# Kernel tuning notes

Hardware: AMD Instinct MI355X
Metric: run time of the kernel (lower is better)

Reference implementation:

```python
import jax, jax.numpy as jnp
import numpy as np

N_NODES = 100000
N_EDGES = 1600000
IN_CH = 128
HID_CH = 128


def setup_inputs() -> dict:
    key = jax.random.key(0)
    ks = jax.random.split(key, 10)
    x = jax.random.normal(ks[0], (N_NODES, IN_CH), dtype=jnp.float32)
    edge_index = jax.random.randint(ks[1], (2, N_EDGES), 0, N_NODES, dtype=jnp.int64)
    s1 = 1.0 / np.sqrt(IN_CH)
    s2 = 1.0 / np.sqrt(HID_CH)
    return {
        "x": x,
        "edge_index": edge_index,
        "W1": jax.random.uniform(ks[2], (IN_CH, HID_CH), jnp.float32, -s1, s1),
        "b1": jnp.zeros((HID_CH,), jnp.float32),
        "W2": jax.random.uniform(ks[3], (HID_CH, HID_CH), jnp.float32, -s2, s2),
        "b2": jnp.zeros((HID_CH,), jnp.float32),
        "We": jax.random.uniform(ks[4], (IN_CH, HID_CH), jnp.float32, -s1, s1),
        "be": jax.random.uniform(ks[5], (HID_CH,), jnp.float32, -s1, s1),
        "Wfc": jax.random.uniform(ks[6], (HID_CH, 1), jnp.float32, -s2, s2),
        "bfc": jax.random.uniform(ks[7], (1,), jnp.float32, -s2, s2),
    }


def _gcn_conv(x, src, dst, norm, W, b, n_nodes):
    # PyG GCNConv: linear transform, then normalized scatter-add aggregation, then bias
    h = x @ W                                 # [N, H]
    msg = h[src] * norm[:, None]              # gather + scale  [E+N, H]
    out = jax.ops.segment_sum(msg, dst, num_segments=n_nodes)  # scatter-add [N, H]
    return out + b


def reference(x, edge_index, W1, b1, W2, b2, We, be, Wfc, bfc):
    n = x.shape[0]
    # add self-loops (PyG default add_self_loops=True)
    loop = jnp.arange(n, dtype=edge_index.dtype)
    src = jnp.concatenate([edge_index[0], loop])
    dst = jnp.concatenate([edge_index[1], loop])
    # symmetric degree normalization deg^-1/2 (edge_weight implicitly ones)
    deg = jax.ops.segment_sum(jnp.ones_like(src, dtype=x.dtype), dst, num_segments=n)
    dinv = jnp.where(deg > 0, jax.lax.rsqrt(deg), 0.0)
    norm = dinv[src] * dinv[dst]

    x_conv = jax.nn.relu(_gcn_conv(x, src, dst, norm, W1, b1, n))
    x_fc = jax.nn.relu(x @ We + be)
    h = x_conv + x_fc                          # residual; dropout is identity in eval
    x_conv2 = jax.nn.relu(_gcn_conv(h, src, dst, norm, W2, b2, n))
    h = x_conv2 + h
    # batch is all zeros -> global_mean_pool == mean over all nodes -> [1, H]
    pooled = jnp.mean(h, axis=0, keepdims=True)
    predict = jax.nn.sigmoid(pooled @ Wfc + bfc)  # [1, 1]
    return predict
```

## Files before the change

kernel.cpp:

```cpp
#include <hip/hip_runtime.h>
#include <hip/hip_bf16.h>

typedef unsigned int uint;
typedef unsigned short ushort;
typedef unsigned char uchar;
typedef __attribute__((ext_vector_type(8))) short short8;
typedef __attribute__((ext_vector_type(4))) float f32x4;
typedef __attribute__((ext_vector_type(4))) uint u32x4;

__device__ __forceinline__ float bf2f(ushort u) {
    union { uint i; float f; } v; v.i = ((uint)u) << 16; return v.f;
}
__device__ __forceinline__ ushort f2bf(float f) {
    union { float f; uint i; } v; v.f = f;
    uint x = v.i;
    uint r = (x + 0x7FFFu + ((x >> 16) & 1u)) >> 16;
    return (ushort)r;
}
__device__ __forceinline__ uchar f2q(float f) {
    return (uchar)(__builtin_amdgcn_cvt_pk_fp8_f32(f, 0.f, 0, false) & 0xFF);
}
__device__ __forceinline__ void q2f4(uint w, float* o) {
    o[0] = __builtin_amdgcn_cvt_f32_fp8(w, 0);
    o[1] = __builtin_amdgcn_cvt_f32_fp8(w, 1);
    o[2] = __builtin_amdgcn_cvt_f32_fp8(w, 2);
    o[3] = __builtin_amdgcn_cvt_f32_fp8(w, 3);
}


__global__ void k_degree(const int* __restrict__ dst, int* __restrict__ deg,
                         int e, int n) {
    int bin = blockIdx.x & 7;
    int sub = blockIdx.x >> 3;
    int nsub = gridDim.x >> 3;
    int q = (n + 7) >> 3;
    int lo = bin * q, hi = min(n, lo + q);
    for (int i = sub * 256 + threadIdx.x; i < e; i += nsub * 256) {
        int d = dst[i];
        if (d >= lo && d < hi) atomicAdd(&deg[d], 1);
    }
}

__global__ void k_dinv(const int* __restrict__ deg, float* __restrict__ dinv, int n) {
    int i = blockIdx.x * 256 + threadIdx.x;
    if (i < n) dinv[i] = rsqrtf((float)deg[i] + 1.0f);
}

__global__ void k_scan_a(const int* __restrict__ deg, int* __restrict__ bsum, int n) {
    __shared__ int sd[256];
    int t = threadIdx.x;
    int base = blockIdx.x * 1024 + t * 4;
    int s = 0;
#pragma unroll
    for (int j = 0; j < 4; ++j) { int idx = base + j; if (idx < n) s += deg[idx]; }
    sd[t] = s; __syncthreads();
    for (int off = 1; off < 256; off <<= 1) {
        int v = (t >= off) ? sd[t - off] : 0;
        __syncthreads();
        sd[t] += v;
        __syncthreads();
    }
    if (t == 255) bsum[blockIdx.x] = sd[255];
}

__global__ void k_scan_b(const int* __restrict__ bsum, int* __restrict__ boff, int nb) {
    __shared__ int sd[256];
    int t = threadIdx.x;
    int v0 = (t < nb) ? bsum[t] : 0;
    sd[t] = v0; __syncthreads();
    for (int off = 1; off < 256; off <<= 1) {
        int v = (t >= off) ? sd[t - off] : 0;
        __syncthreads();
        sd[t] += v;
        __syncthreads();
    }
    if (t < nb) boff[t] = sd[t] - v0;
}

__global__ void k_scan_c(const int* __restrict__ deg, const int* __restrict__ boff,
                         int* __restrict__ offs, int n) {
    __shared__ int sd[256];
    int t = threadIdx.x;
    int base = blockIdx.x * 1024 + t * 4;
    int vals[4]; int s = 0;
#pragma unroll
    for (int j = 0; j < 4; ++j) {
        int idx = base + j;
        vals[j] = (idx < n) ? deg[idx] : 0;
        s += vals[j];
    }
    sd[t] = s; __syncthreads();
    for (int off = 1; off < 256; off <<= 1) {
        int v = (t >= off) ? sd[t - off] : 0;
        __syncthreads();
        sd[t] += v;
        __syncthreads();
    }
    int run = boff[blockIdx.x] + (sd[t] - s);
#pragma unroll
    for (int j = 0; j < 4; ++j) {
        int idx = base + j;
        if (idx < n) { offs[idx] = run; run += vals[j]; }
    }
}

__global__ void k_fill(const int* __restrict__ src, const int* __restrict__ dst,
                       const int* __restrict__ offs, int* __restrict__ cursor,
                       int* __restrict__ csr, int e, int n) {
    int bin = blockIdx.x & 7;
    int sub = blockIdx.x >> 3;
    int nsub = gridDim.x >> 3;
    int q = (n + 7) >> 3;
    int lo = bin * q, hi = min(n, lo + q);
    for (int i = sub * 256 + threadIdx.x; i < e; i += nsub * 256) {
        int d = dst[i];
        if (d >= lo && d < hi) {
            int p = offs[d] + atomicAdd(&cursor[d], 1);
            csr[p] = src[i];
        }
    }
}


__global__ __launch_bounds__(512) void k_gemm1(
    const float* __restrict__ x, const float* __restrict__ W1, const float* __restrict__ We,
    const float* __restrict__ be, const float* __restrict__ dinv,
    uchar* __restrict__ h1q, ushort* __restrict__ xfc, int n)
{
    __shared__ __align__(16) ushort Bt[256][72];
    int tid = threadIdx.x;
    int w = tid >> 6, lane = tid & 63;
    int ln15 = lane & 15, g = lane >> 4;
    int rowBase = blockIdx.x * 128 + w * 16;
    int r = rowBase + ln15;
    bool valid = r < n;

    short8 a[4];
#pragma unroll
    for (int ks = 0; ks < 4; ++ks) {
        float4 f0 = make_float4(0.f, 0.f, 0.f, 0.f), f1 = f0;
        if (valid) {
            const float* p = x + (size_t)r * 128 + ks * 32 + g * 8;
            f0 = *reinterpret_cast<const float4*>(p);
            f1 = *reinterpret_cast<const float4*>(p + 4);
        }
        short8 v;
        v[0] = (short)f2bf(f0.x); v[1] = (short)f2bf(f0.y);
        v[2] = (short)f2bf(f0.z); v[3] = (short)f2bf(f0.w);
        v[4] = (short)f2bf(f1.x); v[5] = (short)f2bf(f1.y);
        v[6] = (short)f2bf(f1.z); v[7] = (short)f2bf(f1.w);
        a[ks] = v;
    }

    f32x4 acc[16];
#pragma unroll
    for (int i = 0; i < 16; ++i) acc[i] = (f32x4){0.f, 0.f, 0.f, 0.f};

    for (int s = 0; s < 2; ++s) {
        for (int i = tid; i < 8192; i += 512) {
            int kl = i >> 7, j = i & 127;
            int kg = s * 64 + kl;
            Bt[j][kl]       = f2bf(W1[kg * 128 + j]);
            Bt[128 + j][kl] = f2bf(We[kg * 128 + j]);
        }
        __syncthreads();
#pragma unroll
        for (int t2 = 0; t2 < 2; ++t2) {
            short8 af = a[s * 2 + t2];
#pragma unroll
            for (int jf = 0; jf < 16; ++jf) {
                short8 bf = *reinterpret_cast<const short8*>(&Bt[jf * 16 + ln15][t2 * 32 + g * 8]);
                acc[jf] = __builtin_amdgcn_mfma_f32_16x16x32_bf16(af, bf, acc[jf], 0, 0, 0);
            }
        }
        __syncthreads();
    }

    float dv[4];
#pragma unroll
    for (int q = 0; q < 4; ++q) {
        int rr = rowBase + g * 4 + q;
        dv[q] = (rr < n) ? dinv[rr] : 0.f;
    }

#pragma unroll
    for (int jf = 0; jf < 16; ++jf) {
        int col = jf * 16 + ln15;
#pragma unroll
        for (int q = 0; q < 4; ++q) {
            int rr = rowBase + g * 4 + q;
            if (rr < n) {
                float v = acc[jf][q];
                if (col < 128) {
                    h1q[(size_t)rr * 128 + col] = f2q(v * dv[q]);
                } else {
                    float vv = fmaxf(v + be[col - 128], 0.f);
                    xfc[(size_t)rr * 128 + (col - 128)] = f2bf(vv);
                }
            }
        }
    }
}


__global__ __launch_bounds__(512) void k_gemm2(
    const ushort* __restrict__ h, const float* __restrict__ W2, const float* __restrict__ dinv,
    uchar* __restrict__ h2q, int n)
{
    __shared__ __align__(16) ushort Bt[128][72];
    int tid = threadIdx.x;
    int w = tid >> 6, lane = tid & 63;
    int ln15 = lane & 15, g = lane >> 4;
    int rowBase = blockIdx.x * 128 + w * 16;
    int r = rowBase + ln15;
    bool valid = r < n;

    short8 a[4];
#pragma unroll
    for (int ks = 0; ks < 4; ++ks) {
        short8 v = (short8){0,0,0,0,0,0,0,0};
        if (valid) v = *reinterpret_cast<const short8*>(h + (size_t)r * 128 + ks * 32 + g * 8);
        a[ks] = v;
    }

    f32x4 acc[8];
#pragma unroll
    for (int i = 0; i < 8; ++i) acc[i] = (f32x4){0.f, 0.f, 0.f, 0.f};

    for (int s = 0; s < 2; ++s) {
        for (int i = tid; i < 8192; i += 512) {
            int kl = i >> 7, j = i & 127;
            Bt[j][kl] = f2bf(W2[(s * 64 + kl) * 128 + j]);
        }
        __syncthreads();
#pragma unroll
        for (int t2 = 0; t2 < 2; ++t2) {
            short8 af = a[s * 2 + t2];
#pragma unroll
            for (int jf = 0; jf < 8; ++jf) {
                short8 bf = *reinterpret_cast<const short8*>(&Bt[jf * 16 + ln15][t2 * 32 + g * 8]);
                acc[jf] = __builtin_amdgcn_mfma_f32_16x16x32_bf16(af, bf, acc[jf], 0, 0, 0);
            }
        }
        __syncthreads();
    }

    float dv[4];
#pragma unroll
    for (int q = 0; q < 4; ++q) {
        int rr = rowBase + g * 4 + q;
        dv[q] = (rr < n) ? dinv[rr] : 0.f;
    }

#pragma unroll
    for (int jf = 0; jf < 8; ++jf) {
        int col = jf * 16 + ln15;
#pragma unroll
        for (int q = 0; q < 4; ++q) {
            int rr = rowBase + g * 4 + q;
            if (rr < n) h2q[(size_t)rr * 128 + col] = f2q(acc[jf][q] * dv[q]);
        }
    }
}


__global__ __launch_bounds__(256) void k_agg1(
    const int* __restrict__ csr, const int* __restrict__ offs, const int* __restrict__ degE,
    const float* __restrict__ dinv, const uchar* __restrict__ h1q, const ushort* __restrict__ xfc,
    const float* __restrict__ b1, ushort* __restrict__ h, int n)
{
    int t = threadIdx.x;
    int g = t >> 3, li = t & 7;
    int node = blockIdx.x * 32 + g;
    if (node >= n) return;
    int off = offs[node], cnt = degE[node];
    float di = dinv[node];
    int c0 = li * 16;
    const uchar* tbl = h1q + c0;
    float acc[16];
#pragma unroll
    for (int e = 0; e < 16; ++e) acc[e] = 0.f;

    for (int base = 0; base < cnt; base += 16) {
        int idx[16];
#pragma unroll
        for (int q = 0; q < 16; ++q) {
            int s = csr[off + base + q];
            idx[q] = (base + q < cnt) ? s : n;
        }
        u32x4 u[16];
#pragma unroll
        for (int q = 0; q < 16; ++q)
            u[q] = *reinterpret_cast<const u32x4*>(tbl + (size_t)idx[q] * 128);
#pragma unroll
        for (int q = 0; q < 16; ++q) {
            float d4[4];
            q2f4(u[q][0], d4); acc[0] += d4[0]; acc[1] += d4[1]; acc[2] += d4[2]; acc[3] += d4[3];
            q2f4(u[q][1], d4); acc[4] += d4[0]; acc[5] += d4[1]; acc[6] += d4[2]; acc[7] += d4[3];
            q2f4(u[q][2], d4); acc[8] += d4[0]; acc[9] += d4[1]; acc[10] += d4[2]; acc[11] += d4[3];
            q2f4(u[q][3], d4); acc[12] += d4[0]; acc[13] += d4[1]; acc[14] += d4[2]; acc[15] += d4[3];
        }
    }

    u32x4 us = *reinterpret_cast<const u32x4*>(tbl + (size_t)node * 128);
    float sdec[16];
    q2f4(us[0], sdec); q2f4(us[1], sdec + 4); q2f4(us[2], sdec + 8); q2f4(us[3], sdec + 12);
    const u32x4* xp = reinterpret_cast<const u32x4*>(xfc + (size_t)node * 128 + c0);
    u32x4 x0 = xp[0], x1 = xp[1];
    uint xw[8] = {x0[0], x0[1], x0[2], x0[3], x1[0], x1[1], x1[2], x1[3]};
    float bb[16];
#pragma unroll
    for (int p = 0; p < 4; ++p) {
        float4 bq = *reinterpret_cast<const float4*>(b1 + c0 + p * 4);
        bb[4 * p] = bq.x; bb[4 * p + 1] = bq.y; bb[4 * p + 2] = bq.z; bb[4 * p + 3] = bq.w;
    }
    uint outw[8];
#pragma unroll
    for (int j = 0; j < 8; ++j) {
        int e0 = 2 * j, e1 = 2 * j + 1;
        float v0 = fmaxf((acc[e0] + sdec[e0]) * di + bb[e0], 0.f) + bf2f((ushort)(xw[j] & 0xffff));
        float v1 = fmaxf((acc[e1] + sdec[e1]) * di + bb[e1], 0.f) + bf2f((ushort)(xw[j] >> 16));
        outw[j] = (uint)f2bf(v0) | ((uint)f2bf(v1) << 16);
    }
    ushort* hp = h + (size_t)node * 128 + c0;
    u32x4 o0 = {outw[0], outw[1], outw[2], outw[3]};
    u32x4 o1 = {outw[4], outw[5], outw[6], outw[7]};
    *reinterpret_cast<u32x4*>(hp) = o0;
    *reinterpret_cast<u32x4*>(hp + 8) = o1;
}


__global__ __launch_bounds__(256) void k_agg2(
    const int* __restrict__ csr, const int* __restrict__ offs, const int* __restrict__ degE,
    const float* __restrict__ dinv, const uchar* __restrict__ h2q, const ushort* __restrict__ hres,
    const float* __restrict__ b2, float* __restrict__ pooled, int n)
{
    __shared__ float lpool[128];
    int t = threadIdx.x;
    if (t < 128) lpool[t] = 0.f;
    __syncthreads();
    int g = t >> 3, li = t & 7;
    int node = blockIdx.x * 32 + g;
    bool valid = node < n;
    int nodeC = valid ? node : (n - 1);
    int off = offs[nodeC];
    int cnt = valid ? degE[nodeC] : 0;
    float di = dinv[nodeC];
    int c0 = li * 16;
    const uchar* tbl = h2q + c0;
    float acc[16];
#pragma unroll
    for (int e = 0; e < 16; ++e) acc[e] = 0.f;

    for (int base = 0; base < cnt; base += 16) {
        int idx[16];
#pragma unroll
        for (int q = 0; q < 16; ++q) {
            int s = csr[off + base + q];
            idx[q] = (base + q < cnt) ? s : n;
        }
        u32x4 u[16];
#pragma unroll
        for (int q = 0; q < 16; ++q)
            u[q] = *reinterpret_cast<const u32x4*>(tbl + (size_t)idx[q] * 128);
#pragma unroll
        for (int q = 0; q < 16; ++q) {
            float d4[4];
            q2f4(u[q][0], d4); acc[0] += d4[0]; acc[1] += d4[1]; acc[2] += d4[2]; acc[3] += d4[3];
            q2f4(u[q][1], d4); acc[4] += d4[0]; acc[5] += d4[1]; acc[6] += d4[2]; acc[7] += d4[3];
            q2f4(u[q][2], d4); acc[8] += d4[0]; acc[9] += d4[1]; acc[10] += d4[2]; acc[11] += d4[3];
            q2f4(u[q][3], d4); acc[12] += d4[0]; acc[13] += d4[1]; acc[14] += d4[2]; acc[15] += d4[3];
        }
    }

    u32x4 us = *reinterpret_cast<const u32x4*>(tbl + (size_t)nodeC * 128);
    float sdec[16];
    q2f4(us[0], sdec); q2f4(us[1], sdec + 4); q2f4(us[2], sdec + 8); q2f4(us[3], sdec + 12);
    const u32x4* rp = reinterpret_cast<const u32x4*>(hres + (size_t)nodeC * 128 + c0);
    u32x4 r0 = rp[0], r1 = rp[1];
    uint rw[8] = {r0[0], r0[1], r0[2], r0[3], r1[0], r1[1], r1[2], r1[3]};
    float bb[16];
#pragma unroll
    for (int p = 0; p < 4; ++p) {
        float4 bq = *reinterpret_cast<const float4*>(b2 + c0 + p * 4);
        bb[4 * p] = bq.x; bb[4 * p + 1] = bq.y; bb[4 * p + 2] = bq.z; bb[4 * p + 3] = bq.w;
    }
    if (valid) {
#pragma unroll
        for (int j = 0; j < 8; ++j) {
            int e0 = 2 * j, e1 = 2 * j + 1;
            float v0 = fmaxf((acc[e0] + sdec[e0]) * di + bb[e0], 0.f) + bf2f((ushort)(rw[j] & 0xffff));
            float v1 = fmaxf((acc[e1] + sdec[e1]) * di + bb[e1], 0.f) + bf2f((ushort)(rw[j] >> 16));
            atomicAdd(&lpool[c0 + e0], v0);
            atomicAdd(&lpool[c0 + e1], v1);
        }
    }
    __syncthreads();
    if (t < 128) atomicAdd(&pooled[t], lpool[t]);
}


__global__ void k_final(const float* __restrict__ pooled, const float* __restrict__ Wfc,
                        const float* __restrict__ bfc, float* __restrict__ out, float invN) {
    int lane = threadIdx.x;
    float s = pooled[2 * lane] * invN * Wfc[2 * lane] +
              pooled[2 * lane + 1] * invN * Wfc[2 * lane + 1];
#pragma unroll
    for (int off = 32; off > 0; off >>= 1) s += __shfl_down(s, off);
    if (lane == 0) out[0] = 1.f / (1.f + expf(-(s + bfc[0])));
}


extern "C" void kernel_launch(void* const* d_in, const int* in_sizes, int n_in,
                              void* d_out, int out_size, void* d_ws, size_t ws_size,
                              hipStream_t stream) {
    const float* x   = (const float*)d_in[0];
    const int*   ei  = (const int*)d_in[1];
    const float* W1  = (const float*)d_in[2];
    const float* b1  = (const float*)d_in[3];
    const float* W2  = (const float*)d_in[4];
    const float* b2  = (const float*)d_in[5];
    const float* We  = (const float*)d_in[6];
    const float* be  = (const float*)d_in[7];
    const float* Wfc = (const float*)d_in[8];
    const float* bfc = (const float*)d_in[9];
    float* out = (float*)d_out;

    const int N = in_sizes[0] / 128;
    const int E = in_sizes[1] / 2;
    const int* src = ei;
    const int* dst = ei + E;

    char* w = (char*)d_ws;
    size_t off = 0;
    auto take = [&](size_t bytes) -> void* {
        void* p = w + off;
        off = (off + bytes + 255) & ~(size_t)255;
        return p;
    };
    int*    deg    = (int*)take((size_t)N * 4);
    int*    offs   = (int*)take((size_t)N * 4);
    int*    cursor = (int*)take((size_t)N * 4);
    float*  dinv   = (float*)take((size_t)N * 4);
    int*    bsum   = (int*)take(1024);
    int*    boff   = (int*)take(1024);
    int*    csr    = (int*)take((size_t)(E + 64) * 4);
    uchar*  h1q    = (uchar*)take((size_t)(N + 1) * 128);
    ushort* xfc    = (ushort*)take((size_t)N * 128 * 2);
    ushort* h      = (ushort*)take((size_t)N * 128 * 2);
    uchar*  h2q    = (uchar*)take((size_t)(N + 1) * 128);
    float*  pooled = (float*)take(512);

    const int nbScan = (N + 1023) / 1024;

    hipMemsetAsync(deg, 0, (size_t)N * 4, stream);
    hipMemsetAsync(cursor, 0, (size_t)N * 4, stream);
    hipMemsetAsync(pooled, 0, 512, stream);
    hipMemsetAsync(h1q + (size_t)N * 128, 0, 128, stream);
    hipMemsetAsync(h2q + (size_t)N * 128, 0, 128, stream);

    k_degree<<<2048, 256, 0, stream>>>(dst, deg, E, N);
    k_dinv<<<(N + 255) / 256, 256, 0, stream>>>(deg, dinv, N);
    k_scan_a<<<nbScan, 256, 0, stream>>>(deg, bsum, N);
    k_scan_b<<<1, 256, 0, stream>>>(bsum, boff, nbScan);
    k_scan_c<<<nbScan, 256, 0, stream>>>(deg, boff, offs, N);
    k_fill<<<2048, 256, 0, stream>>>(src, dst, offs, cursor, csr, E, N);

    k_gemm1<<<(N + 127) / 128, 512, 0, stream>>>(x, W1, We, be, dinv, h1q, xfc, N);
    k_agg1<<<(N + 31) / 32, 256, 0, stream>>>(csr, offs, deg, dinv, h1q, xfc, b1, h, N);
    k_gemm2<<<(N + 127) / 128, 512, 0, stream>>>(h, W2, dinv, h2q, N);
    k_agg2<<<(N + 31) / 32, 256, 0, stream>>>(csr, offs, deg, dinv, h2q, h, b2, pooled, N);
    k_final<<<1, 64, 0, stream>>>(pooled, Wfc, bfc, out, 1.0f / (float)N);
}
```

Baseline: 423.6 us.

## Sort nodes by degree for load-balanced aggregation and fuse memsets into init kernel

Adds a degree histogram, a scan and a scatter that build a degree-sorted node order. Both aggregation kernels then process nodes in that order, so the 8-thread groups in a wavefront have similar edge counts and less divergence. The gather batch drops from 16 to 8 neighbours, and the five memsets are replaced by one init kernel. The cost is three extra small launches, scattered output writes, and less memory-level parallelism per batch.

```diff
diff --git a/kernel.cpp b/kernel.cpp
--- a/kernel.cpp
+++ b/kernel.cpp
@@ -25,6 +25,21 @@
     o[1] = __builtin_amdgcn_cvt_f32_fp8(w, 1);
     o[2] = __builtin_amdgcn_cvt_f32_fp8(w, 2);
     o[3] = __builtin_amdgcn_cvt_f32_fp8(w, 3);
+}
+
+
+__global__ void k_init(int* __restrict__ deg, int* __restrict__ cursor,
+                       int* __restrict__ hist, int* __restrict__ cursB,
+                       float* __restrict__ pooled,
+                       uchar* __restrict__ h1qN, uchar* __restrict__ h2qN, int n) {
+    int i = blockIdx.x * 256 + threadIdx.x;
+    if (i < n) { deg[i] = 0; cursor[i] = 0; }
+    if (i < 64) { hist[i] = 0; cursB[i] = 0; }
+    if (i < 128) pooled[i] = 0.f;
+    if (i < 32) {
+        reinterpret_cast<uint*>(h1qN)[i] = 0;
+        reinterpret_cast<uint*>(h2qN)[i] = 0;
+    }
 }
 
 
@@ -122,6 +137,36 @@
 }
 
 
+__global__ void k_hist(const int* __restrict__ deg, int* __restrict__ hist, int n) {
+    int i = blockIdx.x * 256 + threadIdx.x;
+    if (i < n) atomicAdd(&hist[min(deg[i], 63)], 1);
+}
+
+__global__ void k_sortscan(const int* __restrict__ hist, int* __restrict__ base) {
+    __shared__ int sd[64];
+    int t = threadIdx.x;
+    int v0 = hist[t];
+    sd[t] = v0; __syncthreads();
+    for (int off = 1; off < 64; off <<= 1) {
+        int v = (t >= off) ? sd[t - off] : 0;
+        __syncthreads();
+        sd[t] += v;
+        __syncthreads();
+    }
+    base[t] = sd[t] - v0;
+}
+
+__global__ void k_scatter(const int* __restrict__ deg, const int* __restrict__ base,
+                          int* __restrict__ cursB, int* __restrict__ order, int n) {
+    int i = blockIdx.x * 256 + threadIdx.x;
+    if (i < n) {
+        int b = min(deg[i], 63);
+        int pos = base[b] + atomicAdd(&cursB[b], 1);
+        order[pos] = i;
+    }
+}
+
+
 __global__ __launch_bounds__(512) void k_gemm1(
     const float* __restrict__ x, const float* __restrict__ W1, const float* __restrict__ We,
     const float* __restrict__ be, const float* __restrict__ dinv,
@@ -267,12 +312,13 @@
 __global__ __launch_bounds__(256) void k_agg1(
     const int* __restrict__ csr, const int* __restrict__ offs, const int* __restrict__ degE,
     const float* __restrict__ dinv, const uchar* __restrict__ h1q, const ushort* __restrict__ xfc,
-    const float* __restrict__ b1, ushort* __restrict__ h, int n)
+    const float* __restrict__ b1, ushort* __restrict__ h, const int* __restrict__ order, int n)
 {
     int t = threadIdx.x;
     int g = t >> 3, li = t & 7;
-    int node = blockIdx.x * 32 + g;
-    if (node >= n) return;
+    int j = blockIdx.x * 32 + g;
+    if (j >= n) return;
+    int node = order[j];
     int off = offs[node], cnt = degE[node];
     float di = dinv[node];
     int c0 = li * 16;
@@ -281,19 +327,16 @@
 #pragma unroll
     for (int e = 0; e < 16; ++e) acc[e] = 0.f;
 
-    for (int base = 0; base < cnt; base += 16) {
-        int idx[16];
-#pragma unroll
-        for (int q = 0; q < 16; ++q) {
+    for (int base = 0; base < cnt; base += 8) {
+        u32x4 u[8];
+#pragma unroll
+        for (int q = 0; q < 8; ++q) {
             int s = csr[off + base + q];
-            idx[q] = (base + q < cnt) ? s : n;
-        }
-        u32x4 u[16];
-#pragma unroll
-        for (int q = 0; q < 16; ++q)
-            u[q] = *reinterpret_cast<const u32x4*>(tbl + (size_t)idx[q] * 128);
-#pragma unroll
-        for (int q = 0; q < 16; ++q) {
+            int id = (base + q < cnt) ? s : n;
+            u[q] = *reinterpret_cast<const u32x4*>(tbl + (size_t)id * 128);
+        }
+#pragma unroll
+        for (int q = 0; q < 8; ++q) {
             float d4[4];
             q2f4(u[q][0], d4); acc[0] += d4[0]; acc[1] += d4[1]; acc[2] += d4[2]; acc[3] += d4[3];
             q2f4(u[q][1], d4); acc[4] += d4[0]; acc[5] += d4[1]; acc[6] += d4[2]; acc[7] += d4[3];
@@ -316,11 +359,11 @@
     }
     uint outw[8];
 #pragma unroll
-    for (int j = 0; j < 8; ++j) {
-        int e0 = 2 * j, e1 = 2 * j + 1;
-        float v0 = fmaxf((acc[e0] + sdec[e0]) * di + bb[e0], 0.f) + bf2f((ushort)(xw[j] & 0xffff));
-        float v1 = fmaxf((acc[e1] + sdec[e1]) * di + bb[e1], 0.f) + bf2f((ushort)(xw[j] >> 16));
-        outw[j] = (uint)f2bf(v0) | ((uint)f2bf(v1) << 16);
+    for (int jj = 0; jj < 8; ++jj) {
+        int e0 = 2 * jj, e1 = 2 * jj + 1;
+        float v0 = fmaxf((acc[e0] + sdec[e0]) * di + bb[e0], 0.f) + bf2f((ushort)(xw[jj] & 0xffff));
+        float v1 = fmaxf((acc[e1] + sdec[e1]) * di + bb[e1], 0.f) + bf2f((ushort)(xw[jj] >> 16));
+        outw[jj] = (uint)f2bf(v0) | ((uint)f2bf(v1) << 16);
     }
     ushort* hp = h + (size_t)node * 128 + c0;
     u32x4 o0 = {outw[0], outw[1], outw[2], outw[3]};
@@ -333,38 +376,35 @@
 __global__ __launch_bounds__(256) void k_agg2(
     const int* __restrict__ csr, const int* __restrict__ offs, const int* __restrict__ degE,
     const float* __restrict__ dinv, const uchar* __restrict__ h2q, const ushort* __restrict__ hres,
-    const float* __restrict__ b2, float* __restrict__ pooled, int n)
+    const float* __restrict__ b2, float* __restrict__ pooled, const int* __restrict__ order, int n)
 {
     __shared__ float lpool[128];
     int t = threadIdx.x;
     if (t < 128) lpool[t] = 0.f;
     __syncthreads();
     int g = t >> 3, li = t & 7;
-    int node = blockIdx.x * 32 + g;
-    bool valid = node < n;
-    int nodeC = valid ? node : (n - 1);
-    int off = offs[nodeC];
-    int cnt = valid ? degE[nodeC] : 0;
-    float di = dinv[nodeC];
+    int j = blockIdx.x * 32 + g;
+    bool valid = j < n;
+    int node = valid ? order[j] : 0;
+    int off = offs[node];
+    int cnt = valid ? degE[node] : 0;
+    float di = dinv[node];
     int c0 = li * 16;
     const uchar* tbl = h2q + c0;
     float acc[16];
 #pragma unroll
     for (int e = 0; e < 16; ++e) acc[e] = 0.f;
 
-    for (int base = 0; base < cnt; base += 16) {
-        int idx[16];
-#pragma unroll
-        for (int q = 0; q < 16; ++q) {
+    for (int base = 0; base < cnt; base += 8) {
+        u32x4 u[8];
+#pragma unroll
+        for (int q = 0; q < 8; ++q) {
             int s = csr[off + base + q];
-            idx[q] = (base + q < cnt) ? s : n;
-        }
-        u32x4 u[16];
-#pragma unroll
-        for (int q = 0; q < 16; ++q)
-            u[q] = *reinterpret_cast<const u32x4*>(tbl + (size_t)idx[q] * 128);
-#pragma unroll
-        for (int q = 0; q < 16; ++q) {
+            int id = (base + q < cnt) ? s : n;
+            u[q] = *reinterpret_cast<const u32x4*>(tbl + (size_t)id * 128);
+        }
+#pragma unroll
+        for (int q = 0; q < 8; ++q) {
             float d4[4];
             q2f4(u[q][0], d4); acc[0] += d4[0]; acc[1] += d4[1]; acc[2] += d4[2]; acc[3] += d4[3];
             q2f4(u[q][1], d4); acc[4] += d4[0]; acc[5] += d4[1]; acc[6] += d4[2]; acc[7] += d4[3];
@@ -373,10 +413,10 @@
         }
     }
 
-    u32x4 us = *reinterpret_cast<const u32x4*>(tbl + (size_t)nodeC * 128);
+    u32x4 us = *reinterpret_cast<const u32x4*>(tbl + (size_t)node * 128);
     float sdec[16];
     q2f4(us[0], sdec); q2f4(us[1], sdec + 4); q2f4(us[2], sdec + 8); q2f4(us[3], sdec + 12);
-    const u32x4* rp = reinterpret_cast<const u32x4*>(hres + (size_t)nodeC * 128 + c0);
+    const u32x4* rp = reinterpret_cast<const u32x4*>(hres + (size_t)node * 128 + c0);
     u32x4 r0 = rp[0], r1 = rp[1];
     uint rw[8] = {r0[0], r0[1], r0[2], r0[3], r1[0], r1[1], r1[2], r1[3]};
     float bb[16];
@@ -387,10 +427,10 @@
     }
     if (valid) {
 #pragma unroll
-        for (int j = 0; j < 8; ++j) {
-            int e0 = 2 * j, e1 = 2 * j + 1;
-            float v0 = fmaxf((acc[e0] + sdec[e0]) * di + bb[e0], 0.f) + bf2f((ushort)(rw[j] & 0xffff));
-            float v1 = fmaxf((acc[e1] + sdec[e1]) * di + bb[e1], 0.f) + bf2f((ushort)(rw[j] >> 16));
+        for (int jj = 0; jj < 8; ++jj) {
+            int e0 = 2 * jj, e1 = 2 * jj + 1;
+            float v0 = fmaxf((acc[e0] + sdec[e0]) * di + bb[e0], 0.f) + bf2f((ushort)(rw[jj] & 0xffff));
+            float v1 = fmaxf((acc[e1] + sdec[e1]) * di + bb[e1], 0.f) + bf2f((ushort)(rw[jj] >> 16));
             atomicAdd(&lpool[c0 + e0], v0);
             atomicAdd(&lpool[c0 + e1], v1);
         }
@@ -442,33 +482,37 @@
     int*    offs   = (int*)take((size_t)N * 4);
     int*    cursor = (int*)take((size_t)N * 4);
     float*  dinv   = (float*)take((size_t)N * 4);
+    int*    order  = (int*)take((size_t)N * 4);
     int*    bsum   = (int*)take(1024);
     int*    boff   = (int*)take(1024);
+    int*    hist   = (int*)take(256);
+    int*    sbase  = (int*)take(256);
+    int*    cursB  = (int*)take(256);
+    float*  pooled = (float*)take(512);
     int*    csr    = (int*)take((size_t)(E + 64) * 4);
     uchar*  h1q    = (uchar*)take((size_t)(N + 1) * 128);
     ushort* xfc    = (ushort*)take((size_t)N * 128 * 2);
     ushort* h      = (ushort*)take((size_t)N * 128 * 2);
     uchar*  h2q    = (uchar*)take((size_t)(N + 1) * 128);
-    float*  pooled = (float*)take(512);
 
     const int nbScan = (N + 1023) / 1024;
-
-    hipMemsetAsync(deg, 0, (size_t)N * 4, stream);
-    hipMemsetAsync(cursor, 0, (size_t)N * 4, stream);
-    hipMemsetAsync(pooled, 0, 512, stream);
-    hipMemsetAsync(h1q + (size_t)N * 128, 0, 128, stream);
-    hipMemsetAsync(h2q + (size_t)N * 128, 0, 128, stream);
-
+    const int nbN = (N + 255) / 256;
+
+    k_init<<<nbN, 256, 0, stream>>>(deg, cursor, hist, cursB, pooled,
+                                    h1q + (size_t)N * 128, h2q + (size_t)N * 128, N);
     k_degree<<<2048, 256, 0, stream>>>(dst, deg, E, N);
-    k_dinv<<<(N + 255) / 256, 256, 0, stream>>>(deg, dinv, N);
+    k_dinv<<<nbN, 256, 0, stream>>>(deg, dinv, N);
     k_scan_a<<<nbScan, 256, 0, stream>>>(deg, bsum, N);
     k_scan_b<<<1, 256, 0, stream>>>(bsum, boff, nbScan);
     k_scan_c<<<nbScan, 256, 0, stream>>>(deg, boff, offs, N);
     k_fill<<<2048, 256, 0, stream>>>(src, dst, offs, cursor, csr, E, N);
+    k_hist<<<nbN, 256, 0, stream>>>(deg, hist, N);
+    k_sortscan<<<1, 64, 0, stream>>>(hist, sbase);
+    k_scatter<<<nbN, 256, 0, stream>>>(deg, sbase, cursB, order, N);
 
     k_gemm1<<<(N + 127) / 128, 512, 0, stream>>>(x, W1, We, be, dinv, h1q, xfc, N);
-    k_agg1<<<(N + 31) / 32, 256, 0, stream>>>(csr, offs, deg, dinv, h1q, xfc, b1, h, N);
+    k_agg1<<<(N + 31) / 32, 256, 0, stream>>>(csr, offs, deg, dinv, h1q, xfc, b1, h, order, N);
     k_gemm2<<<(N + 127) / 128, 512, 0, stream>>>(h, W2, dinv, h2q, N);
-    k_agg2<<<(N + 31) / 32, 256, 0, stream>>>(csr, offs, deg, dinv, h2q, h, b2, pooled, N);
+    k_agg2<<<(N + 31) / 32, 256, 0, stream>>>(csr, offs, deg, dinv, h2q, h, b2, pooled, order, N);
     k_final<<<1, 64, 0, stream>>>(pooled, Wfc, bfc, out, 1.0f / (float)N);
 }
```

After: 927.1 us. 119% more time.
